# Optimization experiments

Measured on AMD Instinct MI355X. Metric: run time of the kernel, lower is better.

Reference implementation:

```python
import jax, jax.numpy as jnp
import numpy as np

NUM_HEADS = 8
SCALE = 1.0
BN_EPS = 1e-5


def _mlp1d(x, W1, g1, b1, W2):
    # Conv1d(k=1, bias=False) -> BatchNorm1d (training-mode batch stats) -> ReLU -> Conv1d(k=1, bias=False)
    h = jnp.einsum('oi,bil->bol', W1, x)
    mu = h.mean(axis=(0, 2), keepdims=True)
    var = h.var(axis=(0, 2), keepdims=True)  # biased var, as torch BN training
    h = (h - mu) * jax.lax.rsqrt(var + BN_EPS)
    h = jax.nn.relu(h * g1[None, :, None] + b1[None, :, None])
    return jnp.einsum('oi,bil->bol', W2, h)


def setup_inputs() -> dict:
    key = jax.random.key(0)
    ks = jax.random.split(key, 8)
    b, c, hh, ww = 64, 2048, 14, 14
    hid, out = 4096, 256
    d = {'x': jax.random.normal(ks[0], (b, c, hh, ww), jnp.float32)}

    def w(k, o, i):
        return jax.random.normal(k, (o, i), jnp.float32) * np.float32(1.0 / np.sqrt(i))

    i = 1
    for pre in ('p', 'pp', 'po'):  # proj, proj_pixel, proj_obj
        d[pre + 'W1'] = w(ks[i], hid, c); i += 1
        d[pre + 'G1'] = jnp.ones((hid,), jnp.float32)
        d[pre + 'B1'] = jnp.zeros((hid,), jnp.float32)
        d[pre + 'W2'] = w(ks[i], out, hid); i += 1
    return d


def reference(x, pW1, pG1, pB1, pW2, ppW1, ppG1, ppB1, ppW2, poW1, poG1, poB1, poW2):
    b, c, h, w = x.shape
    xf = x.reshape(b, c, h * w)                      # flatten(2)
    x_pool = xf.mean(axis=2, keepdims=True)          # adaptive_avg_pool2d(x, 1)
    z_g = _mlp1d(x_pool, pW1, pG1, pB1, pW2)         # [b, 256, 1]
    z_feat = _mlp1d(xf, ppW1, ppG1, ppB1, ppW2)      # [b, 256, hw]
    # F.normalize(dim=1) with eps=1e-12, then /scale
    nrm = jnp.maximum(jnp.linalg.norm(z_feat, axis=1, keepdims=True), 1e-12)
    attn = (z_feat / nrm) / SCALE
    attn = attn.reshape(b, NUM_HEADS, -1, h * w)     # [b, nh, 256/nh, hw]
    attn = jax.nn.softmax(attn, axis=-1)
    x4 = xf.reshape(b, NUM_HEADS, c // NUM_HEADS, h * w)
    # torch.matmul(x, obj_attn.transpose(3, 2)) : [b,nh,c/nh,hw] @ [b,nh,hw,q]
    obj_val = jnp.einsum('bnkl,bnql->bnkq', x4, attn).reshape(b, c, -1)  # [b, c, 256/nh]
    obj_val = _mlp1d(obj_val, poW1, poG1, poB1, poW2)                    # [b, 256, 32]
    return z_g, obj_val
```

## Files before the change

kernel.cpp:

```cpp
#include <hip/hip_runtime.h>
#include <hip/hip_bf16.h>

using bf16 = __hip_bfloat16;
typedef __bf16 bf16x8v __attribute__((ext_vector_type(8)));
typedef float f32x4 __attribute__((ext_vector_type(4)));

#define BN_EPS 1e-5f

__device__ __forceinline__ void stval(float* p, float v) { *p = v; }
__device__ __forceinline__ void stval(bf16* p, float v)  { *p = __float2bfloat16(v); }

__device__ __forceinline__ void gload_lds16(const void* g, void* l) {
    __builtin_amdgcn_global_load_lds(
        (const __attribute__((address_space(1))) unsigned int*)g,
        (__attribute__((address_space(3))) unsigned int*)l,
        16, 0, 0);
}

template<typename TC>
__global__ __launch_bounds__(512, 2) void mfma_tn8(
    const bf16* __restrict__ A, const bf16* __restrict__ B, TC* __restrict__ C,
    int M, int N, int K, float* __restrict__ ps, float* __restrict__ pq)
{
    __shared__ char lds[131072];
    const int NT = K >> 6;
    const int tid = threadIdx.x;
    const int lane = tid & 63;
    const int wv = tid >> 6;
    const int wm = wv >> 2;
    const int wn = wv & 3;

    const int nbx = gridDim.x;
    int flat = blockIdx.y * nbx + blockIdx.x;
    const int cpx = (nbx * gridDim.y) >> 3;
    flat = (flat & 7) * cpx + (flat >> 3);
    const int mtile = flat / nbx;
    const long m0 = (long)mtile * 256;
    const long n0 = (long)(flat % nbx) * 256;

    const int trow = tid >> 3;
    const int ks = (((tid & 7) ^ ((tid >> 3) & 7)) << 3);
    const bf16* Arow0 = A + (m0 + trow) * (long)K + ks;
    const bf16* Brow0 = B + (n0 + trow) * (long)K + ks;
    char* ldsA = (char*)lds + tid * 16;
    char* ldsB = (char*)lds + 32768 + tid * 16;

    auto stage_a = [&](int bbuf, int kt) {
        const bf16* g = Arow0 + ((long)kt << 6);
        char* d = ldsA + (bbuf << 16);
        gload_lds16(g, d);
        gload_lds16(g + ((long)K << 6),  d + 8192);
        gload_lds16(g + ((long)K << 7),  d + 16384);
        gload_lds16(g + 192L * (long)K,  d + 24576);
    };
    auto stage_b = [&](int bbuf, int kt) {
        const bf16* g = Brow0 + ((long)kt << 6);
        char* d = ldsB + (bbuf << 16);
        gload_lds16(g, d);
        gload_lds16(g + ((long)K << 6),  d + 8192);
        gload_lds16(g + ((long)K << 7),  d + 16384);
        gload_lds16(g + 192L * (long)K,  d + 24576);
    };

    const int fr = lane & 15, fc = lane >> 4;
    const int ca0 = ((fc ^ (fr & 7)) << 4);
    const int ca1 = (((4 + fc) ^ (fr & 7)) << 4);

    f32x4 acc[8][4];
#pragma unroll
    for (int m = 0; m < 8; ++m)
#pragma unroll
        for (int n = 0; n < 4; ++n) acc[m][n] = (f32x4){0.f, 0.f, 0.f, 0.f};

    stage_a(0, 0); stage_b(0, 0); stage_a(1, 1); stage_b(1, 1);

    for (int T = 0; T < NT; ++T) {
        const int bb = T & 1;
        const char* Ard = (const char*)lds + (bb << 16) + (wm * 128 + fr) * 128;
        const char* Brd = (const char*)lds + (bb << 16) + 32768 + (wn * 64 + fr) * 128;

        if (T == 0)          { asm volatile("s_waitcnt vmcnt(8)" ::: "memory"); }
        else if (T < NT - 1) { asm volatile("s_waitcnt vmcnt(4)" ::: "memory"); }
        else                 { asm volatile("s_waitcnt vmcnt(0)" ::: "memory"); }
        __builtin_amdgcn_s_barrier();
        __builtin_amdgcn_sched_barrier(0);

        bf16x8v a0[8], a1[8];
#pragma unroll
        for (int m = 0; m < 8; ++m) {
            a0[m] = *(const bf16x8v*)(Ard + m * 2048 + ca0);
            a1[m] = *(const bf16x8v*)(Ard + m * 2048 + ca1);
        }
        bf16x8v b00 = *(const bf16x8v*)(Brd + ca0);
        bf16x8v b01 = *(const bf16x8v*)(Brd + ca1);
        bf16x8v b10 = *(const bf16x8v*)(Brd + 2048 + ca0);
        bf16x8v b11 = *(const bf16x8v*)(Brd + 2048 + ca1);

        if (T >= 1 && T + 1 < NT) stage_b(bb ^ 1, T + 1);

        __builtin_amdgcn_s_setprio(1);
#pragma unroll
        for (int m = 0; m < 8; ++m) {
            acc[m][0] = __builtin_amdgcn_mfma_f32_16x16x32_bf16(a0[m], b00, acc[m][0], 0, 0, 0);
            acc[m][0] = __builtin_amdgcn_mfma_f32_16x16x32_bf16(a1[m], b01, acc[m][0], 0, 0, 0);
            acc[m][1] = __builtin_amdgcn_mfma_f32_16x16x32_bf16(a0[m], b10, acc[m][1], 0, 0, 0);
            acc[m][1] = __builtin_amdgcn_mfma_f32_16x16x32_bf16(a1[m], b11, acc[m][1], 0, 0, 0);
        }
        __builtin_amdgcn_s_setprio(0);

        __builtin_amdgcn_s_barrier();
        __builtin_amdgcn_sched_barrier(0);

        bf16x8v b20 = *(const bf16x8v*)(Brd + 2 * 2048 + ca0);
        bf16x8v b21 = *(const bf16x8v*)(Brd + 2 * 2048 + ca1);
        bf16x8v b30 = *(const bf16x8v*)(Brd + 3 * 2048 + ca0);
        bf16x8v b31 = *(const bf16x8v*)(Brd + 3 * 2048 + ca1);

        if (T + 2 < NT) stage_a(bb, T + 2);

        __builtin_amdgcn_s_setprio(1);
#pragma unroll
        for (int m = 0; m < 8; ++m) {
            acc[m][2] = __builtin_amdgcn_mfma_f32_16x16x32_bf16(a0[m], b20, acc[m][2], 0, 0, 0);
            acc[m][2] = __builtin_amdgcn_mfma_f32_16x16x32_bf16(a1[m], b21, acc[m][2], 0, 0, 0);
            acc[m][3] = __builtin_amdgcn_mfma_f32_16x16x32_bf16(a0[m], b30, acc[m][3], 0, 0, 0);
            acc[m][3] = __builtin_amdgcn_mfma_f32_16x16x32_bf16(a1[m], b31, acc[m][3], 0, 0, 0);
        }
        __builtin_amdgcn_s_setprio(0);
    }

#pragma unroll
    for (int m = 0; m < 8; ++m) {
        long gr = m0 + wm * 128 + m * 16 + fc * 4;
#pragma unroll
        for (int n = 0; n < 4; ++n) {
            long gc = n0 + wn * 64 + n * 16 + fr;
            TC* cp = C + gr * N + gc;
#pragma unroll
            for (int r = 0; r < 4; ++r) stval(cp + (long)r * N, acc[m][n][r]);
        }
    }

    if (ps != nullptr) {
        __syncthreads();
        float* red = (float*)lds;
        float cs[4], cq[4];
#pragma unroll
        for (int n = 0; n < 4; ++n) {
            float s = 0.f, q = 0.f;
#pragma unroll
            for (int m = 0; m < 8; ++m)
#pragma unroll
                for (int r = 0; r < 4; ++r) {
                    float v = __bfloat162float(__float2bfloat16(acc[m][n][r]));
                    s += v; q += v * v;
                }
            s += __shfl_xor(s, 16, 64); s += __shfl_xor(s, 32, 64);
            q += __shfl_xor(q, 16, 64); q += __shfl_xor(q, 32, 64);
            cs[n] = s; cq[n] = q;
        }
        if (fc == 0) {
#pragma unroll
            for (int n = 0; n < 4; ++n) {
                red[wv * 64 + n * 16 + fr] = cs[n];
                red[512 + wv * 64 + n * 16 + fr] = cq[n];
            }
        }
        __syncthreads();
        if (tid < 256) {
            int c = tid, wnn = c >> 6, idx = c & 63;
            float s = red[wnn * 64 + idx] + red[(4 + wnn) * 64 + idx];
            float q = red[512 + wnn * 64 + idx] + red[512 + (4 + wnn) * 64 + idx];
            ps[(long)mtile * N + n0 + c] = s;
            pq[(long)mtile * N + n0 + c] = q;
        }
    }
}

template<typename TC>
__global__ __launch_bounds__(256) void mfma_tn(
    const bf16* __restrict__ A, const bf16* __restrict__ B, TC* __restrict__ C,
    int M, int N, int K, float* __restrict__ ps, float* __restrict__ pq)
{
    __shared__ alignas(16) unsigned short As[128 * 32];
    __shared__ alignas(16) unsigned short Bs[128 * 32];

    const int tid = threadIdx.x;
    const int l = tid & 63;
    const long m0 = (long)blockIdx.y * 128;
    const long n0 = (long)blockIdx.x * 128;
    const int wr = (tid >> 7) & 1;
    const int wc = (tid >> 6) & 1;

    const int off0 = tid * 16;
    const int row0 = off0 >> 6;
    const int kp0  = (off0 >> 4) & 3;
    const bf16* Ag0 = A + (m0 + row0) * (long)K + kp0 * 8;
    const bf16* Ag1 = A + (m0 + row0 + 64) * (long)K + kp0 * 8;
    const bf16* Bg0 = B + (n0 + row0) * (long)K + kp0 * 8;
    const bf16* Bg1 = B + (n0 + row0 + 64) * (long)K + kp0 * 8;
    char* Asl0 = (char*)As + off0;
    char* Asl1 = (char*)As + off0 + 4096;
    char* Bsl0 = (char*)Bs + off0;
    char* Bsl1 = (char*)Bs + off0 + 4096;

    f32x4 acc[4][4];
#pragma unroll
    for (int m = 0; m < 4; ++m)
#pragma unroll
        for (int n = 0; n < 4; ++n) acc[m][n] = (f32x4){0.f, 0.f, 0.f, 0.f};

    const int fr = l & 15;
    const int fc = l >> 4;
    int aoff[4], boff[4];
#pragma unroll
    for (int m = 0; m < 4; ++m) aoff[m] = ((wr * 64 + m * 16 + fr) * 4 + fc) * 16;
#pragma unroll
    for (int n = 0; n < 4; ++n) boff[n] = ((wc * 64 + n * 16 + fr) * 4 + fc) * 16;

    for (int k0 = 0; k0 < K; k0 += 32) {
        gload_lds16(Ag0 + k0, Asl0);
        gload_lds16(Ag1 + k0, Asl1);
        gload_lds16(Bg0 + k0, Bsl0);
        gload_lds16(Bg1 + k0, Bsl1);
        __syncthreads();

        bf16x8v af[4], bfr[4];
#pragma unroll
        for (int m = 0; m < 4; ++m) af[m]  = *(const bf16x8v*)((const char*)As + aoff[m]);
#pragma unroll
        for (int n = 0; n < 4; ++n) bfr[n] = *(const bf16x8v*)((const char*)Bs + boff[n]);
#pragma unroll
        for (int m = 0; m < 4; ++m)
#pragma unroll
            for (int n = 0; n < 4; ++n)
                acc[m][n] = __builtin_amdgcn_mfma_f32_16x16x32_bf16(af[m], bfr[n], acc[m][n], 0, 0, 0);
        __syncthreads();
    }

#pragma unroll
    for (int m = 0; m < 4; ++m) {
        long gr = m0 + wr * 64 + m * 16 + fc * 4;
#pragma unroll
        for (int n = 0; n < 4; ++n) {
            long gc = n0 + wc * 64 + n * 16 + fr;
            TC* cp = C + gr * N + gc;
#pragma unroll
            for (int r = 0; r < 4; ++r) stval(cp + (long)r * N, acc[m][n][r]);
        }
    }

    if (ps != nullptr) {
        float* red = (float*)As;
        float cs[4], cq[4];
#pragma unroll
        for (int n = 0; n < 4; ++n) {
            float s = 0.f, q = 0.f;
#pragma unroll
            for (int m = 0; m < 4; ++m)
#pragma unroll
                for (int r = 0; r < 4; ++r) {
                    float v = __bfloat162float(__float2bfloat16(acc[m][n][r]));
                    s += v; q += v * v;
                }
            s += __shfl_xor(s, 16, 64); s += __shfl_xor(s, 32, 64);
            q += __shfl_xor(q, 16, 64); q += __shfl_xor(q, 32, 64);
            cs[n] = s; cq[n] = q;
        }
        if (fc == 0) {
#pragma unroll
            for (int n = 0; n < 4; ++n) {
                int c = wc * 64 + n * 16 + fr;
                red[wr * 128 + c] = cs[n];
                red[256 + wr * 128 + c] = cq[n];
            }
        }
        __syncthreads();
        if (tid < 128) {
            float s = red[tid] + red[128 + tid];
            float q = red[256 + tid] + red[384 + tid];
            ps[(long)blockIdx.y * N + n0 + tid] = s;
            pq[(long)blockIdx.y * N + n0 + tid] = q;
        }
    }
}

__global__ __launch_bounds__(256) void mfma_tn_bn(
    const bf16* __restrict__ A, const bf16* __restrict__ B, float* __restrict__ C,
    int M, int N, int K, const float* __restrict__ ta, const float* __restrict__ tc)
{
    __shared__ alignas(16) unsigned short As[128 * 32];
    __shared__ alignas(16) unsigned short Bs[128 * 32];

    const int tid = threadIdx.x;
    const int l = tid & 63;
    const long m0 = (long)blockIdx.y * 128;
    const long n0 = (long)blockIdx.x * 128;
    const int wr = (tid >> 7) & 1;
    const int wc = (tid >> 6) & 1;

    const int off0 = tid * 16;
    const int row0 = off0 >> 6;
    const int kp0  = (off0 >> 4) & 3;
    const bf16* Ag0 = A + (m0 + row0) * (long)K + kp0 * 8;
    const bf16* Ag1 = A + (m0 + row0 + 64) * (long)K + kp0 * 8;
    const bf16* Bg0 = B + (n0 + row0) * (long)K + kp0 * 8;
    const bf16* Bg1 = B + (n0 + row0 + 64) * (long)K + kp0 * 8;
    char* Asl0 = (char*)As + off0;
    char* Asl1 = (char*)As + off0 + 4096;
    char* Bsl0 = (char*)Bs + off0;
    char* Bsl1 = (char*)Bs + off0 + 4096;

    f32x4 acc[4][4];
#pragma unroll
    for (int m = 0; m < 4; ++m)
#pragma unroll
        for (int n = 0; n < 4; ++n) acc[m][n] = (f32x4){0.f, 0.f, 0.f, 0.f};

    const int fr = l & 15;
    const int fc = l >> 4;
    int aoff[4], boff[4];
#pragma unroll
    for (int m = 0; m < 4; ++m) aoff[m] = ((wr * 64 + m * 16 + fr) * 4 + fc) * 16;
#pragma unroll
    for (int n = 0; n < 4; ++n) boff[n] = ((wc * 64 + n * 16 + fr) * 4 + fc) * 16;

    for (int k0 = 0; k0 < K; k0 += 32) {
        gload_lds16(Bg0 + k0, Bsl0);
        gload_lds16(Bg1 + k0, Bsl1);

        union { bf16 h[8]; uint4 u; } r0, r1;
        r0.u = *(const uint4*)(Ag0 + k0);
        r1.u = *(const uint4*)(Ag1 + k0);
        const int kb = k0 + kp0 * 8;
        float4 av0 = *(const float4*)(ta + kb);
        float4 av1 = *(const float4*)(ta + kb + 4);
        float4 cv0 = *(const float4*)(tc + kb);
        float4 cv1 = *(const float4*)(tc + kb + 4);
        float av[8] = {av0.x, av0.y, av0.z, av0.w, av1.x, av1.y, av1.z, av1.w};
        float cv[8] = {cv0.x, cv0.y, cv0.z, cv0.w, cv1.x, cv1.y, cv1.z, cv1.w};
#pragma unroll
        for (int j = 0; j < 8; ++j) {
            float v = fmaxf(fmaf(av[j], __bfloat162float(r0.h[j]), cv[j]), 0.f);
            r0.h[j] = __float2bfloat16(v);
            v = fmaxf(fmaf(av[j], __bfloat162float(r1.h[j]), cv[j]), 0.f);
            r1.h[j] = __float2bfloat16(v);
        }
        *(uint4*)Asl0 = r0.u;
        *(uint4*)Asl1 = r1.u;
        __syncthreads();

        bf16x8v af[4], bfr[4];
#pragma unroll
        for (int m = 0; m < 4; ++m) af[m]  = *(const bf16x8v*)((const char*)As + aoff[m]);
#pragma unroll
        for (int n = 0; n < 4; ++n) bfr[n] = *(const bf16x8v*)((const char*)Bs + boff[n]);
#pragma unroll
        for (int m = 0; m < 4; ++m)
#pragma unroll
            for (int n = 0; n < 4; ++n)
                acc[m][n] = __builtin_amdgcn_mfma_f32_16x16x32_bf16(af[m], bfr[n], acc[m][n], 0, 0, 0);
        __syncthreads();
    }

#pragma unroll
    for (int m = 0; m < 4; ++m) {
        long gr = m0 + wr * 64 + m * 16 + fc * 4;
#pragma unroll
        for (int n = 0; n < 4; ++n) {
            long gc = n0 + wc * 64 + n * 16 + fr;
            float* cp = C + gr * N + gc;
#pragma unroll
            for (int r = 0; r < 4; ++r) cp[(long)r * N] = acc[m][n][r];
        }
    }
}

__global__ __launch_bounds__(256) void mfma_tn_skbn(
    const bf16* __restrict__ A, const bf16* __restrict__ B, float* __restrict__ Cp,
    int M, int N, int K, int KCH, const float* __restrict__ ta, const float* __restrict__ tc)
{
    __shared__ alignas(16) unsigned short As[128 * 32];
    __shared__ alignas(16) unsigned short Bs[128 * 32];

    const int tid = threadIdx.x;
    const int l = tid & 63;
    const long m0 = (long)blockIdx.y * 128;
    const long n0 = (long)blockIdx.x * 128;
    const int wr = (tid >> 7) & 1;
    const int wc = (tid >> 6) & 1;
    const int ksrt = blockIdx.z * KCH;

    const int off0 = tid * 16;
    const int row0 = off0 >> 6;
    const int kp0  = (off0 >> 4) & 3;
    const bf16* Ag0 = A + (m0 + row0) * (long)K + kp0 * 8 + ksrt;
    const bf16* Ag1 = A + (m0 + row0 + 64) * (long)K + kp0 * 8 + ksrt;
    const bf16* Bg0 = B + (n0 + row0) * (long)K + kp0 * 8 + ksrt;
    const bf16* Bg1 = B + (n0 + row0 + 64) * (long)K + kp0 * 8 + ksrt;
    char* Asl0 = (char*)As + off0;
    char* Asl1 = (char*)As + off0 + 4096;
    char* Bsl0 = (char*)Bs + off0;
    char* Bsl1 = (char*)Bs + off0 + 4096;

    f32x4 acc[4][4];
#pragma unroll
    for (int m = 0; m < 4; ++m)
#pragma unroll
        for (int n = 0; n < 4; ++n) acc[m][n] = (f32x4){0.f, 0.f, 0.f, 0.f};

    const int fr = l & 15;
    const int fc = l >> 4;
    int aoff[4], boff[4];
#pragma unroll
    for (int m = 0; m < 4; ++m) aoff[m] = ((wr * 64 + m * 16 + fr) * 4 + fc) * 16;
#pragma unroll
    for (int n = 0; n < 4; ++n) boff[n] = ((wc * 64 + n * 16 + fr) * 4 + fc) * 16;

    for (int k0 = 0; k0 < KCH; k0 += 32) {
        gload_lds16(Bg0 + k0, Bsl0);
        gload_lds16(Bg1 + k0, Bsl1);

        union { bf16 h[8]; uint4 u; } r0, r1;
        r0.u = *(const uint4*)(Ag0 + k0);
        r1.u = *(const uint4*)(Ag1 + k0);
        const int kb = ksrt + k0 + kp0 * 8;
        float4 av0 = *(const float4*)(ta + kb);
        float4 av1 = *(const float4*)(ta + kb + 4);
        float4 cv0 = *(const float4*)(tc + kb);
        float4 cv1 = *(const float4*)(tc + kb + 4);
        float av[8] = {av0.x, av0.y, av0.z, av0.w, av1.x, av1.y, av1.z, av1.w};
        float cv[8] = {cv0.x, cv0.y, cv0.z, cv0.w, cv1.x, cv1.y, cv1.z, cv1.w};
#pragma unroll
        for (int j = 0; j < 8; ++j) {
            float v = fmaxf(fmaf(av[j], __bfloat162float(r0.h[j]), cv[j]), 0.f);
            r0.h[j] = __float2bfloat16(v);
            v = fmaxf(fmaf(av[j], __bfloat162float(r1.h[j]), cv[j]), 0.f);
            r1.h[j] = __float2bfloat16(v);
        }
        *(uint4*)Asl0 = r0.u;
        *(uint4*)Asl1 = r1.u;
        __syncthreads();

        bf16x8v af[4], bfr[4];
#pragma unroll
        for (int m = 0; m < 4; ++m) af[m]  = *(const bf16x8v*)((const char*)As + aoff[m]);
#pragma unroll
        for (int n = 0; n < 4; ++n) bfr[n] = *(const bf16x8v*)((const char*)Bs + boff[n]);
#pragma unroll
        for (int m = 0; m < 4; ++m)
#pragma unroll
            for (int n = 0; n < 4; ++n)
                acc[m][n] = __builtin_amdgcn_mfma_f32_16x16x32_bf16(af[m], bfr[n], acc[m][n], 0, 0, 0);
        __syncthreads();
    }

    float* Cb = Cp + (long)blockIdx.z * M * N;
#pragma unroll
    for (int m = 0; m < 4; ++m) {
        long gr = m0 + wr * 64 + m * 16 + fc * 4;
#pragma unroll
        for (int n = 0; n < 4; ++n) {
            long gc = n0 + wc * 64 + n * 16 + fr;
            float* cp = Cb + gr * N + gc;
#pragma unroll
            for (int r = 0; r < 4; ++r) cp[(long)r * N] = acc[m][n][r];
        }
    }
}

__global__ __launch_bounds__(256) void objmm_k(
    const bf16* __restrict__ attnP, const bf16* __restrict__ xP, bf16* __restrict__ objinT)
{
    __shared__ alignas(16) unsigned short As[32 * 32];
    __shared__ alignas(16) unsigned short Bs[256 * 32];
    const int tid = threadIdx.x, lane = tid & 63, wv = tid >> 6;
    const int b = blockIdx.x >> 3, h = blockIdx.x & 7;
    const bf16* Ab = attnP + ((long)(b * 256 + h * 32)) * 224;
    const bf16* Bb = xP + ((long)(b * 2048 + h * 256)) * 224;
    const int fr = lane & 15, fc = lane >> 4;
    const int srow = tid >> 2, schk = tid & 3;

    f32x4 acc[2][4];
#pragma unroll
    for (int m = 0; m < 2; ++m)
#pragma unroll
        for (int n = 0; n < 4; ++n) acc[m][n] = (f32x4){0.f, 0.f, 0.f, 0.f};

    for (int k0 = 0; k0 < 224; k0 += 32) {
        if (wv < 2)
            gload_lds16(Ab + (long)srow * 224 + schk * 8 + k0, (char*)As + tid * 16);
#pragma unroll
        for (int j = 0; j < 4; ++j)
            gload_lds16(Bb + (long)(j * 64 + srow) * 224 + schk * 8 + k0,
                        (char*)Bs + j * 4096 + tid * 16);
        __syncthreads();

        bf16x8v af[2], bfr[4];
#pragma unroll
        for (int m = 0; m < 2; ++m)
            af[m] = *(const bf16x8v*)((const char*)As + (m * 16 + fr) * 64 + fc * 16);
#pragma unroll
        for (int n = 0; n < 4; ++n)
            bfr[n] = *(const bf16x8v*)((const char*)Bs + (wv * 64 + n * 16 + fr) * 64 + fc * 16);
#pragma unroll
        for (int m = 0; m < 2; ++m)
#pragma unroll
            for (int n = 0; n < 4; ++n)
                acc[m][n] = __builtin_amdgcn_mfma_f32_16x16x32_bf16(af[m], bfr[n], acc[m][n], 0, 0, 0);
        __syncthreads();
    }

#pragma unroll
    for (int m = 0; m < 2; ++m) {
        long gr = (long)b * 32 + m * 16 + fc * 4;
#pragma unroll
        for (int n = 0; n < 4; ++n) {
            long gc = (long)h * 256 + wv * 64 + n * 16 + fr;
            bf16* cp = objinT + gr * 2048 + gc;
#pragma unroll
            for (int r = 0; r < 4; ++r) cp[(long)r * 2048] = __float2bfloat16(acc[m][n][r]);
        }
    }
}

__global__ __launch_bounds__(256) void foldout_k(const float* __restrict__ p, float* __restrict__ out)
{
    int o = blockIdx.x * 256 + threadIdx.x;
    int b = o >> 13, rem = o & 8191, q = rem >> 5, tt = rem & 31;
    long base = ((long)(b * 32 + tt)) * 256 + q;
    float s = p[base] + p[524288 + base] + p[2 * 524288 + base] + p[3 * 524288 + base];
    out[o] = s;
}

__global__ __launch_bounds__(256) void convert4_k(
    const float* __restrict__ w1, const float* __restrict__ w2,
    const float* __restrict__ w3, const float* __restrict__ w4,
    bf16* __restrict__ o1, bf16* __restrict__ o2,
    bf16* __restrict__ o3, bf16* __restrict__ o4)
{
    const long L1 = 8388608, L2 = 1048576;
    long i = ((long)blockIdx.x * 256 + threadIdx.x) * 8;
    const float* src; bf16* dst; long e;
    if (i < L1)                { src = w1; dst = o1; e = i; }
    else if (i < L1 + L2)      { src = w2; dst = o2; e = i - L1; }
    else if (i < 2*L1 + L2)    { src = w3; dst = o3; e = i - L1 - L2; }
    else if (i < 2*L1 + 2*L2)  { src = w4; dst = o4; e = i - 2*L1 - L2; }
    else return;
    float4 v0 = *(const float4*)(src + e);
    float4 v1 = *(const float4*)(src + e + 4);
    union { bf16 h[8]; uint4 u; } r;
    r.h[0] = __float2bfloat16(v0.x); r.h[1] = __float2bfloat16(v0.y);
    r.h[2] = __float2bfloat16(v0.z); r.h[3] = __float2bfloat16(v0.w);
    r.h[4] = __float2bfloat16(v1.x); r.h[5] = __float2bfloat16(v1.y);
    r.h[6] = __float2bfloat16(v1.z); r.h[7] = __float2bfloat16(v1.w);
    *(uint4*)(dst + e) = r.u;
}

__global__ __launch_bounds__(256) void packx2_k(const float* __restrict__ x,
    bf16* __restrict__ XT, bf16* __restrict__ xP, float* __restrict__ xpT)
{
    __shared__ unsigned short tile[196 * 66 + 4];
    __shared__ float pp[64];
    const int t = threadIdx.x;
    const int b = blockIdx.y, c0 = blockIdx.x * 64;
    const int wvi = t >> 6, lane = t & 63;

    for (int p = 0; p < 16; ++p) {
        int c = p * 4 + wvi;
        const float* row = x + ((long)b * 2048 + c0 + c) * 196;
        float v0 = row[lane];
        float v1 = row[lane + 64];
        float v2 = row[lane + 128];
        float v3 = (lane < 4) ? row[lane + 192] : 0.f;
        bf16 h0 = __float2bfloat16(v0);
        bf16 h1 = __float2bfloat16(v1);
        bf16 h2 = __float2bfloat16(v2);
        bf16 h3 = __float2bfloat16(v3);
        tile[lane * 66 + c]         = *(unsigned short*)&h0;
        tile[(lane + 64) * 66 + c]  = *(unsigned short*)&h1;
        tile[(lane + 128) * 66 + c] = *(unsigned short*)&h2;
        if (lane < 4) tile[(lane + 192) * 66 + c] = *(unsigned short*)&h3;
        float s = v0 + v1 + v2 + v3;
#pragma unroll
        for (int off = 32; off; off >>= 1) s += __shfl_xor(s, off, 64);
        if (lane == 0) pp[c] = s;
    }
    __syncthreads();
    if (t < 64) xpT[(c0 + t) * 64 + b] = pp[t] * (1.f / 196.f);

    for (int u = t; u < 196 * 8; u += 256) {
        int l = u >> 3, cc = u & 7;
        const unsigned short* sp = &tile[l * 66 + cc * 8];
        uint4 r;
        r.x = *(const unsigned int*)(sp);
        r.y = *(const unsigned int*)(sp + 2);
        r.z = *(const unsigned int*)(sp + 4);
        r.w = *(const unsigned int*)(sp + 6);
        *(uint4*)(&XT[((long)b * 196 + l) * 2048 + c0 + cc * 8]) = r;
    }

    for (int u = t; u < 64 * 28; u += 256) {
        int c = u / 28, ch = u % 28;
        int l0 = ch * 8;
        union { unsigned short h[8]; uint4 v; } r;
#pragma unroll
        for (int e = 0; e < 8; ++e) {
            int ll = l0 + e;
            r.h[e] = (ll < 196) ? tile[ll * 66 + c] : (unsigned short)0;
        }
        *(uint4*)(xP + ((long)b * 2048 + c0 + c) * 224 + l0) = r.v;
    }
}

__global__ __launch_bounds__(256) void colstat2_k(const float* __restrict__ ps, const float* __restrict__ pq,
    int P, float invN, const float* __restrict__ g, const float* __restrict__ be,
    float* __restrict__ ta, float* __restrict__ tc)
{
    int c = blockIdx.x * 256 + threadIdx.x;
    float s = 0.f, q = 0.f;
    for (int p = 0; p < P; ++p) { s += ps[(long)p * 4096 + c]; q += pq[(long)p * 4096 + c]; }
    float mu  = s * invN;
    float var = q * invN - mu * mu;
    float a   = g[c] * rsqrtf(var + BN_EPS);
    ta[c] = a;
    tc[c] = be[c] - mu * a;
}

__global__ __launch_bounds__(256) void norm2_k(const float* __restrict__ z, float* __restrict__ invn, int J)
{
    int j = blockIdx.x * 4 + (threadIdx.x >> 6);
    int l = threadIdx.x & 63;
    if (j >= J) return;
    const float* row = z + (long)j * 256;
    float s = 0.f;
#pragma unroll
    for (int i = 0; i < 4; ++i) { float v = row[l + 64 * i]; s += v * v; }
#pragma unroll
    for (int off = 32; off; off >>= 1) s += __shfl_xor(s, off, 64);
    if (l == 0) invn[j] = 1.f / fmaxf(sqrtf(s), 1e-12f);
}

__global__ __launch_bounds__(256) void softmax2_k(const float* __restrict__ z,
    const float* __restrict__ invn, bf16* __restrict__ attnP)
{
    int row  = blockIdx.x * 4 + (threadIdx.x >> 6);
    int lane = threadIdx.x & 63;
    int b = row >> 8, q = row & 255;
    float v[4];
    float mx = -INFINITY;
#pragma unroll
    for (int i = 0; i < 4; ++i) {
        int l = lane + 64 * i;
        if (l < 196) {
            int j = b * 196 + l;
            v[i] = z[(long)j * 256 + q] * invn[j];
        } else v[i] = -INFINITY;
        mx = fmaxf(mx, v[i]);
    }
#pragma unroll
    for (int off = 32; off; off >>= 1) mx = fmaxf(mx, __shfl_xor(mx, off, 64));
    float s = 0.f;
#pragma unroll
    for (int i = 0; i < 4; ++i) {
        v[i] = (lane + 64 * i < 196) ? __expf(v[i] - mx) : 0.f;
        s += v[i];
    }
#pragma unroll
    for (int off = 32; off; off >>= 1) s += __shfl_xor(s, off, 64);
    float is = 1.f / s;
    bf16* rp = attnP + (long)row * 224;
#pragma unroll
    for (int i = 0; i < 4; ++i) {
        int l = lane + 64 * i;
        if (l < 196) rp[l] = __float2bfloat16(v[i] * is);
        else if (l < 224) rp[l] = __float2bfloat16(0.f);
    }
}

template<bool TRANS>
__global__ __launch_bounds__(256) void gemmsk_k(
    const float* __restrict__ A, const float* __restrict__ B, float* __restrict__ Cp,
    int M, int N, int K, int lda, int ldbk, int KCH,
    const float* __restrict__ tra, const float* __restrict__ trc)
{
    constexpr int BM = 64, BN = 64, BK = 16;
    __shared__ float As[BK][BM + 4];
    __shared__ float Bs[BK][BN + 4];

    const int tid = threadIdx.x;
    const int m0 = blockIdx.y * BM;
    const int ks = blockIdx.z * KCH;
    const int ke = min(K, ks + KCH);

    const int tIdm = tid / 16;
    const int tIdn = tid % 16;
    const int aK  = tid % BK;
    const int aM0 = tid / BK;
    const int bN  = tid % BN;
    const int bK0 = tid / BN;

    float acc[4][4];
#pragma unroll
    for (int u = 0; u < 4; ++u)
#pragma unroll
        for (int v = 0; v < 4; ++v) acc[u][v] = 0.f;

    for (int k0 = ks; k0 < ke; k0 += BK) {
#pragma unroll
        for (int i = 0; i < 4; ++i) {
            int m = aM0 + 16 * i;
            int gk = k0 + aK, gm = m0 + m;
            float v = 0.f;
            if (gk < ke && gm < M) v = A[(long)gm * lda + gk];
            As[aK][m] = v;
        }
#pragma unroll
        for (int i = 0; i < 4; ++i) {
            int kk = bK0 + 4 * i;
            int gk = k0 + kk;
            float v = 0.f;
            if (gk < ke && bN < N) {
                v = B[(long)gk * ldbk + bN];
                if (TRANS) v = fmaxf(tra[gk] * v + trc[gk], 0.f);
            }
            Bs[kk][bN] = v;
        }
        __syncthreads();
#pragma unroll
        for (int kk = 0; kk < BK; ++kk) {
            float a[4], b[4];
#pragma unroll
            for (int u = 0; u < 4; ++u) a[u] = As[kk][tIdm * 4 + u];
#pragma unroll
            for (int v = 0; v < 4; ++v) b[v] = Bs[kk][tIdn * 4 + v];
#pragma unroll
            for (int u = 0; u < 4; ++u)
#pragma unroll
                for (int v = 0; v < 4; ++v)
                    acc[u][v] = fmaf(a[u], b[v], acc[u][v]);
        }
        __syncthreads();
    }

    float* Cb = Cp + (long)blockIdx.z * M * N;
#pragma unroll
    for (int u = 0; u < 4; ++u) {
        int gm = m0 + tIdm * 4 + u;
        if (gm >= M) continue;
#pragma unroll
        for (int v = 0; v < 4; ++v) {
            int gn = tIdn * 4 + v;
            if (gn < N) Cb[(long)gm * N + gn] = acc[u][v];
        }
    }
}

__global__ __launch_bounds__(256) void skbn_k(const float* __restrict__ Cp,
    const float* __restrict__ g, const float* __restrict__ be,
    float* __restrict__ h1, float* __restrict__ ta, float* __restrict__ tc)
{
    int o = blockIdx.x * 4 + (threadIdx.x >> 6);
    int b = threadIdx.x & 63;
    float s = 0.f;
#pragma unroll
    for (int p = 0; p < 16; ++p) s += Cp[(long)p * 262144 + o * 64 + b];
    h1[o * 64 + b] = s;
    float s1 = s, s2 = s * s;
#pragma unroll
    for (int off = 32; off; off >>= 1) {
        s1 += __shfl_down(s1, off, 64);
        s2 += __shfl_down(s2, off, 64);
    }
    if (b == 0) {
        float mu  = s1 * (1.f / 64.f);
        float var = s2 * (1.f / 64.f) - mu * mu;
        float a   = g[o] * rsqrtf(var + BN_EPS);
        ta[o] = a;
        tc[o] = be[o] - mu * a;
    }
}

__global__ __launch_bounds__(256) void skreduce_k(const float* __restrict__ Cp, int P, long MN,
    int Nn, int ldm, int ldn, float* __restrict__ out)
{
    long i = (long)blockIdx.x * 256 + threadIdx.x;
    if (i >= MN) return;
    float s = 0.f;
    for (int p = 0; p < P; ++p) s += Cp[(long)p * MN + i];
    int m = (int)(i / Nn), n = (int)(i % Nn);
    out[(long)m * ldm + (long)n * ldn] = s;
}

extern "C" void kernel_launch(void* const* d_in, const int* in_sizes, int n_in,
                              void* d_out, int out_size, void* d_ws, size_t ws_size,
                              hipStream_t stream)
{
    const float* x    = (const float*)d_in[0];
    const float* pW1  = (const float*)d_in[1];
    const float* pG1  = (const float*)d_in[2];
    const float* pB1  = (const float*)d_in[3];
    const float* pW2  = (const float*)d_in[4];
    const float* ppW1 = (const float*)d_in[5];
    const float* ppG1 = (const float*)d_in[6];
    const float* ppB1 = (const float*)d_in[7];
    const float* ppW2 = (const float*)d_in[8];
    const float* poW1 = (const float*)d_in[9];
    const float* poG1 = (const float*)d_in[10];
    const float* poB1 = (const float*)d_in[11];
    const float* poW2 = (const float*)d_in[12];
    float* out = (float*)d_out;
    (void)in_sizes; (void)n_in; (void)out_size; (void)ws_size;

    char* w = (char*)d_ws;
    auto alloc = [&](size_t bytes) -> char* {
        char* p = w; w += (bytes + 255) & ~(size_t)255; return p;
    };
    bf16* ppW1b = (bf16*)alloc((size_t)4096 * 2048 * 2);
    bf16* ppW2b = (bf16*)alloc((size_t)256 * 4096 * 2);
    bf16* poW1b = (bf16*)alloc((size_t)4096 * 2048 * 2);
    bf16* poW2b = (bf16*)alloc((size_t)256 * 4096 * 2);
    char* region1 = alloc((size_t)12544 * 2048 * 2);
    bf16*  XT     = (bf16*)region1;
    bf16*  attnP  = (bf16*)region1;
    bf16*  objinT = (bf16*)(region1 + 12845056);
    bf16*  hobjT  = (bf16*)(region1 + 12845056 + 8388608);
    bf16* xP     = (bf16*)alloc((size_t)64 * 2048 * 224 * 2);
    bf16* hfeatT = (bf16*)alloc((size_t)12544 * 4096 * 2);
    float* zfeatT = (float*)alloc((size_t)12544 * 256 * 4);
    float* ps    = (float*)alloc((size_t)49 * 4096 * 4);
    float* pq    = (float*)alloc((size_t)49 * 4096 * 4);
    float* invn  = (float*)alloc((size_t)12544 * 4);
    float* a2    = (float*)alloc(4096 * 4);
    float* c2    = (float*)alloc(4096 * 4);
    float* a3    = (float*)alloc(4096 * 4);
    float* c3    = (float*)alloc(4096 * 4);
    float* xpT   = (float*)alloc((size_t)2048 * 64 * 4);
    float* h1    = (float*)alloc((size_t)4096 * 64 * 4);
    float* a1    = (float*)alloc(4096 * 4);
    float* c1    = (float*)alloc(4096 * 4);
    float* skp1  = (float*)alloc((size_t)16 * 4096 * 64 * 4);
    float* skp2  = (float*)alloc((size_t)32 * 256 * 64 * 4);
    float* skp5  = (float*)alloc((size_t)4 * 2048 * 256 * 4);

    convert4_k<<<9216, 256, 0, stream>>>(ppW1, ppW2, poW1, poW2, ppW1b, ppW2b, poW1b, poW2b);
    packx2_k<<<dim3(32, 64), 256, 0, stream>>>(x, XT, xP, xpT);

    gemmsk_k<false><<<dim3(1, 64, 16), 256, 0, stream>>>(
        pW1, xpT, skp1, 4096, 64, 2048, 2048, 64, 128, nullptr, nullptr);
    skbn_k<<<1024, 256, 0, stream>>>(skp1, pG1, pB1, h1, a1, c1);
    gemmsk_k<true><<<dim3(1, 4, 32), 256, 0, stream>>>(
        pW2, h1, skp2, 256, 64, 4096, 4096, 64, 128, a1, c1);
    skreduce_k<<<64, 256, 0, stream>>>(skp2, 32, (long)256 * 64, 64, 1, 256, out);

    mfma_tn8<bf16><<<dim3(16, 49), 512, 0, stream>>>(XT, ppW1b, hfeatT, 12544, 4096, 2048, ps, pq);
    colstat2_k<<<16, 256, 0, stream>>>(ps, pq, 49, 1.f / 12544.f, ppG1, ppB1, a2, c2);

    mfma_tn_bn<<<dim3(2, 98), 256, 0, stream>>>(hfeatT, ppW2b, zfeatT, 12544, 256, 4096, a2, c2);

    norm2_k<<<3136, 256, 0, stream>>>(zfeatT, invn, 12544);
    softmax2_k<<<4096, 256, 0, stream>>>(zfeatT, invn, attnP);

    objmm_k<<<512, 256, 0, stream>>>(attnP, xP, objinT);

    mfma_tn<bf16><<<dim3(32, 16), 256, 0, stream>>>(objinT, poW1b, hobjT, 2048, 4096, 2048, ps, pq);
    colstat2_k<<<16, 256, 0, stream>>>(ps, pq, 16, 1.f / 2048.f, poG1, poB1, a3, c3);

    mfma_tn_skbn<<<dim3(2, 16, 4), 256, 0, stream>>>(hobjT, poW2b, skp5, 2048, 256, 4096, 1024, a3, c3);
    foldout_k<<<2048, 256, 0, stream>>>(skp5, out + 16384);
}
```

Baseline: 688.7 us.

## Triple-buffer A in big GEMM, split-K second GEMM, XCD swizzle smaller GEMMs

The main 256x256 GEMM now keeps three A buffers and two B buffers in 160KB of LDS. Both prefetches are issued right after a single barrier per k-step, and all 32 MFMAs run in one phase instead of two. This is meant to remove the mid-iteration barrier and overlap loads better. The hfeat x W2 GEMM, which had only 196 blocks, now uses the split-K BN-fused kernel with two K chunks, followed by a new fold kernel that also computes row norms, replacing norm2_k. XCD-aware block swizzling is added to mfma_tn and mfma_tn_skbn to improve L2 locality. The trade-off is more LDS per block, which lowers occupancy, plus an extra partial-sum buffer pass.

```diff
diff --git a/kernel.cpp b/kernel.cpp
--- a/kernel.cpp
+++ b/kernel.cpp
@@ -17,12 +17,18 @@
         16, 0, 0);
 }
 
+__device__ __forceinline__ int xcd_swz(int orig, int nwg) {
+    int q = nwg >> 3, r = nwg & 7;
+    int xcd = orig & 7, idx = orig >> 3;
+    return (xcd < r ? xcd * (q + 1) : r * (q + 1) + (xcd - r) * q) + idx;
+}
+
 template<typename TC>
 __global__ __launch_bounds__(512, 2) void mfma_tn8(
     const bf16* __restrict__ A, const bf16* __restrict__ B, TC* __restrict__ C,
     int M, int N, int K, float* __restrict__ ps, float* __restrict__ pq)
 {
-    __shared__ char lds[131072];
+    __shared__ alignas(16) char lds[163840];
     const int NT = K >> 6;
     const int tid = threadIdx.x;
     const int lane = tid & 63;
@@ -42,12 +48,10 @@
     const int ks = (((tid & 7) ^ ((tid >> 3) & 7)) << 3);
     const bf16* Arow0 = A + (m0 + trow) * (long)K + ks;
     const bf16* Brow0 = B + (n0 + trow) * (long)K + ks;
-    char* ldsA = (char*)lds + tid * 16;
-    char* ldsB = (char*)lds + 32768 + tid * 16;
-
-    auto stage_a = [&](int bbuf, int kt) {
+
+    auto stage_a = [&](int abuf, int kt) {
         const bf16* g = Arow0 + ((long)kt << 6);
-        char* d = ldsA + (bbuf << 16);
+        char* d = (char*)lds + abuf * 32768 + tid * 16;
         gload_lds16(g, d);
         gload_lds16(g + ((long)K << 6),  d + 8192);
         gload_lds16(g + ((long)K << 7),  d + 16384);
@@ -55,7 +59,7 @@
     };
     auto stage_b = [&](int bbuf, int kt) {
         const bf16* g = Brow0 + ((long)kt << 6);
-        char* d = ldsB + (bbuf << 16);
+        char* d = (char*)lds + 98304 + bbuf * 32768 + tid * 16;
         gload_lds16(g, d);
         gload_lds16(g + ((long)K << 6),  d + 8192);
         gload_lds16(g + ((long)K << 7),  d + 16384);
@@ -72,60 +76,42 @@
 #pragma unroll
         for (int n = 0; n < 4; ++n) acc[m][n] = (f32x4){0.f, 0.f, 0.f, 0.f};
 
-    stage_a(0, 0); stage_b(0, 0); stage_a(1, 1); stage_b(1, 1);
+    stage_a(0, 0); stage_b(0, 0); stage_a(1, 1);
 
     for (int T = 0; T < NT; ++T) {
-        const int bb = T & 1;
-        const char* Ard = (const char*)lds + (bb << 16) + (wm * 128 + fr) * 128;
-        const char* Brd = (const char*)lds + (bb << 16) + 32768 + (wn * 64 + fr) * 128;
-
-        if (T == 0)          { asm volatile("s_waitcnt vmcnt(8)" ::: "memory"); }
-        else if (T < NT - 1) { asm volatile("s_waitcnt vmcnt(4)" ::: "memory"); }
-        else                 { asm volatile("s_waitcnt vmcnt(0)" ::: "memory"); }
+        const int aT = T % 3, bT = T & 1;
+
+        if (T < NT - 1) { asm volatile("s_waitcnt vmcnt(4)" ::: "memory"); }
+        else            { asm volatile("s_waitcnt vmcnt(0)" ::: "memory"); }
         __builtin_amdgcn_s_barrier();
         __builtin_amdgcn_sched_barrier(0);
 
-        bf16x8v a0[8], a1[8];
+        if (T + 1 < NT) stage_b((T + 1) & 1, T + 1);
+        if (T + 2 < NT) stage_a((T + 2) % 3, T + 2);
+
+        const char* Ard = (const char*)lds + aT * 32768 + (wm * 128 + fr) * 128;
+        const char* Brd = (const char*)lds + 98304 + bT * 32768 + (wn * 64 + fr) * 128;
+
+        bf16x8v a0[8], a1[8], bl[4], bh[4];
 #pragma unroll
         for (int m = 0; m < 8; ++m) {
             a0[m] = *(const bf16x8v*)(Ard + m * 2048 + ca0);
             a1[m] = *(const bf16x8v*)(Ard + m * 2048 + ca1);
         }
-        bf16x8v b00 = *(const bf16x8v*)(Brd + ca0);
-        bf16x8v b01 = *(const bf16x8v*)(Brd + ca1);
-        bf16x8v b10 = *(const bf16x8v*)(Brd + 2048 + ca0);
-        bf16x8v b11 = *(const bf16x8v*)(Brd + 2048 + ca1);
-
-        if (T >= 1 && T + 1 < NT) stage_b(bb ^ 1, T + 1);
+#pragma unroll
+        for (int n = 0; n < 4; ++n) {
+            bl[n] = *(const bf16x8v*)(Brd + n * 2048 + ca0);
+            bh[n] = *(const bf16x8v*)(Brd + n * 2048 + ca1);
+        }
 
         __builtin_amdgcn_s_setprio(1);
 #pragma unroll
-        for (int m = 0; m < 8; ++m) {
-            acc[m][0] = __builtin_amdgcn_mfma_f32_16x16x32_bf16(a0[m], b00, acc[m][0], 0, 0, 0);
-            acc[m][0] = __builtin_amdgcn_mfma_f32_16x16x32_bf16(a1[m], b01, acc[m][0], 0, 0, 0);
-            acc[m][1] = __builtin_amdgcn_mfma_f32_16x16x32_bf16(a0[m], b10, acc[m][1], 0, 0, 0);
-            acc[m][1] = __builtin_amdgcn_mfma_f32_16x16x32_bf16(a1[m], b11, acc[m][1], 0, 0, 0);
-        }
-        __builtin_amdgcn_s_setprio(0);
-
-        __builtin_amdgcn_s_barrier();
-        __builtin_amdgcn_sched_barrier(0);
-
-        bf16x8v b20 = *(const bf16x8v*)(Brd + 2 * 2048 + ca0);
-        bf16x8v b21 = *(const bf16x8v*)(Brd + 2 * 2048 + ca1);
-        bf16x8v b30 = *(const bf16x8v*)(Brd + 3 * 2048 + ca0);
-        bf16x8v b31 = *(const bf16x8v*)(Brd + 3 * 2048 + ca1);
-
-        if (T + 2 < NT) stage_a(bb, T + 2);
-
-        __builtin_amdgcn_s_setprio(1);
-#pragma unroll
-        for (int m = 0; m < 8; ++m) {
-            acc[m][2] = __builtin_amdgcn_mfma_f32_16x16x32_bf16(a0[m], b20, acc[m][2], 0, 0, 0);
-            acc[m][2] = __builtin_amdgcn_mfma_f32_16x16x32_bf16(a1[m], b21, acc[m][2], 0, 0, 0);
-            acc[m][3] = __builtin_amdgcn_mfma_f32_16x16x32_bf16(a0[m], b30, acc[m][3], 0, 0, 0);
-            acc[m][3] = __builtin_amdgcn_mfma_f32_16x16x32_bf16(a1[m], b31, acc[m][3], 0, 0, 0);
-        }
+        for (int m = 0; m < 8; ++m)
+#pragma unroll
+            for (int n = 0; n < 4; ++n) {
+                acc[m][n] = __builtin_amdgcn_mfma_f32_16x16x32_bf16(a0[m], bl[n], acc[m][n], 0, 0, 0);
+                acc[m][n] = __builtin_amdgcn_mfma_f32_16x16x32_bf16(a1[m], bh[n], acc[m][n], 0, 0, 0);
+            }
         __builtin_amdgcn_s_setprio(0);
     }
 
@@ -187,8 +173,11 @@
 
     const int tid = threadIdx.x;
     const int l = tid & 63;
-    const long m0 = (long)blockIdx.y * 128;
-    const long n0 = (long)blockIdx.x * 128;
+    const int nwg = gridDim.x * gridDim.y;
+    int s = xcd_swz(blockIdx.y * gridDim.x + blockIdx.x, nwg);
+    const int by = s / gridDim.x, bx = s % gridDim.x;
+    const long m0 = (long)by * 128;
+    const long n0 = (long)bx * 128;
     const int wr = (tid >> 7) & 1;
     const int wc = (tid >> 6) & 1;
 
@@ -255,17 +244,17 @@
         float cs[4], cq[4];
 #pragma unroll
         for (int n = 0; n < 4; ++n) {
-            float s = 0.f, q = 0.f;
+            float s2 = 0.f, q2 = 0.f;
 #pragma unroll
             for (int m = 0; m < 4; ++m)
 #pragma unroll
                 for (int r = 0; r < 4; ++r) {
                     float v = __bfloat162float(__float2bfloat16(acc[m][n][r]));
-                    s += v; q += v * v;
+                    s2 += v; q2 += v * v;
                 }
-            s += __shfl_xor(s, 16, 64); s += __shfl_xor(s, 32, 64);
-            q += __shfl_xor(q, 16, 64); q += __shfl_xor(q, 32, 64);
-            cs[n] = s; cq[n] = q;
+            s2 += __shfl_xor(s2, 16, 64); s2 += __shfl_xor(s2, 32, 64);
+            q2 += __shfl_xor(q2, 16, 64); q2 += __shfl_xor(q2, 32, 64);
+            cs[n] = s2; cq[n] = q2;
         }
         if (fc == 0) {
 #pragma unroll
@@ -277,101 +266,10 @@
         }
         __syncthreads();
         if (tid < 128) {
-            float s = red[tid] + red[128 + tid];
-            float q = red[256 + tid] + red[384 + tid];
-            ps[(long)blockIdx.y * N + n0 + tid] = s;
-            pq[(long)blockIdx.y * N + n0 + tid] = q;
-        }
-    }
-}
-
-__global__ __launch_bounds__(256) void mfma_tn_bn(
-    const bf16* __restrict__ A, const bf16* __restrict__ B, float* __restrict__ C,
-    int M, int N, int K, const float* __restrict__ ta, const float* __restrict__ tc)
-{
-    __shared__ alignas(16) unsigned short As[128 * 32];
-    __shared__ alignas(16) unsigned short Bs[128 * 32];
-
-    const int tid = threadIdx.x;
-    const int l = tid & 63;
-    const long m0 = (long)blockIdx.y * 128;
-    const long n0 = (long)blockIdx.x * 128;
-    const int wr = (tid >> 7) & 1;
-    const int wc = (tid >> 6) & 1;
-
-    const int off0 = tid * 16;
-    const int row0 = off0 >> 6;
-    const int kp0  = (off0 >> 4) & 3;
-    const bf16* Ag0 = A + (m0 + row0) * (long)K + kp0 * 8;
-    const bf16* Ag1 = A + (m0 + row0 + 64) * (long)K + kp0 * 8;
-    const bf16* Bg0 = B + (n0 + row0) * (long)K + kp0 * 8;
-    const bf16* Bg1 = B + (n0 + row0 + 64) * (long)K + kp0 * 8;
-    char* Asl0 = (char*)As + off0;
-    char* Asl1 = (char*)As + off0 + 4096;
-    char* Bsl0 = (char*)Bs + off0;
-    char* Bsl1 = (char*)Bs + off0 + 4096;
-
-    f32x4 acc[4][4];
-#pragma unroll
-    for (int m = 0; m < 4; ++m)
-#pragma unroll
-        for (int n = 0; n < 4; ++n) acc[m][n] = (f32x4){0.f, 0.f, 0.f, 0.f};
-
-    const int fr = l & 15;
-    const int fc = l >> 4;
-    int aoff[4], boff[4];
-#pragma unroll
-    for (int m = 0; m < 4; ++m) aoff[m] = ((wr * 64 + m * 16 + fr) * 4 + fc) * 16;
-#pragma unroll
-    for (int n = 0; n < 4; ++n) boff[n] = ((wc * 64 + n * 16 + fr) * 4 + fc) * 16;
-
-    for (int k0 = 0; k0 < K; k0 += 32) {
-        gload_lds16(Bg0 + k0, Bsl0);
-        gload_lds16(Bg1 + k0, Bsl1);
-
-        union { bf16 h[8]; uint4 u; } r0, r1;
-        r0.u = *(const uint4*)(Ag0 + k0);
-        r1.u = *(const uint4*)(Ag1 + k0);
-        const int kb = k0 + kp0 * 8;
-        float4 av0 = *(const float4*)(ta + kb);
-        float4 av1 = *(const float4*)(ta + kb + 4);
-        float4 cv0 = *(const float4*)(tc + kb);
-        float4 cv1 = *(const float4*)(tc + kb + 4);
-        float av[8] = {av0.x, av0.y, av0.z, av0.w, av1.x, av1.y, av1.z, av1.w};
-        float cv[8] = {cv0.x, cv0.y, cv0.z, cv0.w, cv1.x, cv1.y, cv1.z, cv1.w};
-#pragma unroll
-        for (int j = 0; j < 8; ++j) {
-            float v = fmaxf(fmaf(av[j], __bfloat162float(r0.h[j]), cv[j]), 0.f);
-            r0.h[j] = __float2bfloat16(v);
-            v = fmaxf(fmaf(av[j], __bfloat162float(r1.h[j]), cv[j]), 0.f);
-            r1.h[j] = __float2bfloat16(v);
-        }
-        *(uint4*)Asl0 = r0.u;
-        *(uint4*)Asl1 = r1.u;
-        __syncthreads();
-
-        bf16x8v af[4], bfr[4];
-#pragma unroll
-        for (int m = 0; m < 4; ++m) af[m]  = *(const bf16x8v*)((const char*)As + aoff[m]);
-#pragma unroll
-        for (int n = 0; n < 4; ++n) bfr[n] = *(const bf16x8v*)((const char*)Bs + boff[n]);
-#pragma unroll
-        for (int m = 0; m < 4; ++m)
-#pragma unroll
-            for (int n = 0; n < 4; ++n)
-                acc[m][n] = __builtin_amdgcn_mfma_f32_16x16x32_bf16(af[m], bfr[n], acc[m][n], 0, 0, 0);
-        __syncthreads();
-    }
-
-#pragma unroll
-    for (int m = 0; m < 4; ++m) {
-        long gr = m0 + wr * 64 + m * 16 + fc * 4;
-#pragma unroll
-        for (int n = 0; n < 4; ++n) {
-            long gc = n0 + wc * 64 + n * 16 + fr;
-            float* cp = C + gr * N + gc;
-#pragma unroll
-            for (int r = 0; r < 4; ++r) cp[(long)r * N] = acc[m][n][r];
+            float sv = red[tid] + red[128 + tid];
+            float qv = red[256 + tid] + red[384 + tid];
+            ps[(long)by * N + n0 + tid] = sv;
+            pq[(long)by * N + n0 + tid] = qv;
         }
     }
 }
@@ -385,11 +283,17 @@
 
     const int tid = threadIdx.x;
     const int l = tid & 63;
-    const long m0 = (long)blockIdx.y * 128;
-    const long n0 = (long)blockIdx.x * 128;
+    const int gxy = gridDim.x * gridDim.y;
+    const int nwg = gxy * gridDim.z;
+    int s = xcd_swz((blockIdx.z * gridDim.y + blockIdx.y) * gridDim.x + blockIdx.x, nwg);
+    const int bz = s / gxy;
+    const int rem = s % gxy;
+    const int by = rem / gridDim.x, bx = rem % gridDim.x;
+    const long m0 = (long)by * 128;
+    const long n0 = (long)bx * 128;
     const int wr = (tid >> 7) & 1;
     const int wc = (tid >> 6) & 1;
-    const int ksrt = blockIdx.z * KCH;
+    const int ksrt = bz * KCH;
 
     const int off0 = tid * 16;
     const int row0 = off0 >> 6;
@@ -455,7 +359,7 @@
         __syncthreads();
     }
 
-    float* Cb = Cp + (long)blockIdx.z * M * N;
+    float* Cb = Cp + (long)bz * M * N;
 #pragma unroll
     for (int m = 0; m < 4; ++m) {
         long gr = m0 + wr * 64 + m * 16 + fc * 4;
@@ -522,6 +426,21 @@
             for (int r = 0; r < 4; ++r) cp[(long)r * 2048] = __float2bfloat16(acc[m][n][r]);
         }
     }
+}
+
+__global__ __launch_bounds__(256) void foldnorm_k(const float* __restrict__ p,
+    float* __restrict__ z, float* __restrict__ invn)
+{
+    int j = blockIdx.x * 4 + (threadIdx.x >> 6);
+    int lane = threadIdx.x & 63;
+    float4 a = *(const float4*)(p + (long)j * 256 + lane * 4);
+    float4 b = *(const float4*)(p + 3211264L + (long)j * 256 + lane * 4);
+    float4 s; s.x = a.x + b.x; s.y = a.y + b.y; s.z = a.z + b.z; s.w = a.w + b.w;
+    *(float4*)(z + (long)j * 256 + lane * 4) = s;
+    float q = s.x * s.x + s.y * s.y + s.z * s.z + s.w * s.w;
+#pragma unroll
+    for (int off = 32; off; off >>= 1) q += __shfl_xor(q, off, 64);
+    if (lane == 0) invn[j] = 1.f / fmaxf(sqrtf(q), 1e-12f);
 }
 
 __global__ __launch_bounds__(256) void foldout_k(const float* __restrict__ p, float* __restrict__ out)
@@ -625,20 +544,6 @@
     float a   = g[c] * rsqrtf(var + BN_EPS);
     ta[c] = a;
     tc[c] = be[c] - mu * a;
-}
-
-__global__ __launch_bounds__(256) void norm2_k(const float* __restrict__ z, float* __restrict__ invn, int J)
-{
-    int j = blockIdx.x * 4 + (threadIdx.x >> 6);
-    int l = threadIdx.x & 63;
-    if (j >= J) return;
-    const float* row = z + (long)j * 256;
-    float s = 0.f;
-#pragma unroll
-    for (int i = 0; i < 4; ++i) { float v = row[l + 64 * i]; s += v * v; }
-#pragma unroll
-    for (int off = 32; off; off >>= 1) s += __shfl_xor(s, off, 64);
-    if (l == 0) invn[j] = 1.f / fmaxf(sqrtf(s), 1e-12f);
 }
 
 __global__ __launch_bounds__(256) void softmax2_k(const float* __restrict__ z,
@@ -842,6 +747,7 @@
     float* skp1  = (float*)alloc((size_t)16 * 4096 * 64 * 4);
     float* skp2  = (float*)alloc((size_t)32 * 256 * 64 * 4);
     float* skp5  = (float*)alloc((size_t)4 * 2048 * 256 * 4);
+    float* skpG2 = (float*)alloc((size_t)2 * 12544 * 256 * 4);
 
     convert4_k<<<9216, 256, 0, stream>>>(ppW1, ppW2, poW1, poW2, ppW1b, ppW2b, poW1b, poW2b);
     packx2_k<<<dim3(32, 64), 256, 0, stream>>>(x, XT, xP, xpT);
@@ -856,9 +762,10 @@
     mfma_tn8<bf16><<<dim3(16, 49), 512, 0, stream>>>(XT, ppW1b, hfeatT, 12544, 4096, 2048, ps, pq);
     colstat2_k<<<16, 256, 0, stream>>>(ps, pq, 49, 1.f / 12544.f, ppG1, ppB1, a2, c2);
 
-    mfma_tn_bn<<<dim3(2, 98), 256, 0, stream>>>(hfeatT, ppW2b, zfeatT, 12544, 256, 4096, a2, c2);
-
-    norm2_k<<<3136, 256, 0, stream>>>(zfeatT, invn, 12544);
+    mfma_tn_skbn<<<dim3(2, 98, 2), 256, 0, stream>>>(
+        hfeatT, ppW2b, skpG2, 12544, 256, 4096, 2048, a2, c2);
+    foldnorm_k<<<3136, 256, 0, stream>>>(skpG2, zfeatT, invn);
+
     softmax2_k<<<4096, 256, 0, stream>>>(zfeatT, invn, attnP);
 
     objmm_k<<<512, 256, 0, stream>>>(attnP, xP, objinT);
@@ -866,6 +773,7 @@
     mfma_tn<bf16><<<dim3(32, 16), 256, 0, stream>>>(objinT, poW1b, hobjT, 2048, 4096, 2048, ps, pq);
     colstat2_k<<<16, 256, 0, stream>>>(ps, pq, 16, 1.f / 2048.f, poG1, poB1, a3, c3);
 
-    mfma_tn_skbn<<<dim3(2, 16, 4), 256, 0, stream>>>(hobjT, poW2b, skp5, 2048, 256, 4096, 1024, a3, c3);
+    mfma_tn_skbn<<<dim3(2, 16, 4), 256, 0, stream>>>(
+        hobjT, poW2b, skp5, 2048, 256, 4096, 1024, a3, c3);
     foldout_k<<<2048, 256, 0, stream>>>(skp5, out + 16384);
 }
```

After: 639.3 us. 1.08x faster.
